# Kernel optimization log

Measured on AMD Instinct MI355X. Metric: run time of the kernel, lower is better.

Reference implementation:

```python
import jax, jax.numpy as jnp
import numpy as np

COMMITMENT = 0.25
EPS = 1e-12  # F.normalize default eps


def _l2norm(x, axis=-1):
    n = jnp.sqrt(jnp.sum(x * x, axis=axis, keepdims=True))
    return x / jnp.maximum(n, EPS)


def _wn(g, v):
    # torch weight_norm(Linear) with dim=0: per-output-row normalization
    return g[:, None] * v / jnp.maximum(jnp.sqrt(jnp.sum(v * v, axis=1, keepdims=True)), EPS)


def setup_inputs() -> dict:
    key = jax.random.key(0)
    ks = jax.random.split(key, 8)
    B, D, T = 16, 1024, 4096
    CS, CD = 1024, 8
    return {
        "z": jax.random.normal(ks[0], (B, D, T), dtype=jnp.float32),
        "codebook": jax.random.normal(ks[1], (CS, CD), dtype=jnp.float32),
        "g_in": jax.random.uniform(ks[2], (CD,), dtype=jnp.float32) + 0.5,
        "v_in": jax.random.normal(ks[3], (CD, D), dtype=jnp.float32) * 0.02,
        "b_in": jax.random.normal(ks[4], (CD,), dtype=jnp.float32) * 0.02,
        "g_out": jax.random.uniform(ks[5], (D,), dtype=jnp.float32) + 0.5,
        "v_out": jax.random.normal(ks[6], (D, CD), dtype=jnp.float32) * 0.02,
        "b_out": jax.random.normal(ks[7], (D,), dtype=jnp.float32) * 0.02,
    }


def reference(z, codebook, g_in, v_in, b_in, g_out, v_out, b_out):
    B, D, T = z.shape
    CS, CD = codebook.shape
    W_in = _wn(g_in, v_in)    # [CD, D]
    W_out = _wn(g_out, v_out)  # [D, CD]

    # in_proj: (b t d) @ W_in^T + b -> expressed directly on [B, D, T]
    z_e = jnp.einsum("bdt,cd->bct", z, W_in) + b_in[None, :, None]  # [B, CD, T]

    # decode_latents: cosine-distance nearest neighbor over codebook
    enc = z_e.transpose(0, 2, 1).reshape(B * T, CD)
    enc_n = _l2norm(enc)
    cb_n = _l2norm(codebook)
    dist = (
        jnp.sum(enc_n * enc_n, axis=1, keepdims=True)
        - 2.0 * enc_n @ cb_n.T
        + jnp.sum(cb_n * cb_n, axis=1)[None, :]
    )  # [B*T, CS]
    indices = jnp.argmax(-dist, axis=1).reshape(B, T)  # [B, T]

    # gather from the UN-normalized codebook (embed_code uses raw weights)
    z_q = codebook[indices].transpose(0, 2, 1)  # [B, CD, T]

    sg = jax.lax.stop_gradient
    commitment_loss = jnp.mean((z_e - sg(z_q)) ** 2, axis=(1, 2)) * COMMITMENT
    codebook_loss = jnp.mean((z_q - sg(z_e)) ** 2, axis=(1, 2))
    commit_loss = commitment_loss + codebook_loss  # [B]

    # straight-through estimator
    z_q_st = z_e + sg(z_q - z_e)  # [B, CD, T]

    out = jnp.einsum("bct,dc->bdt", z_q_st, W_out) + b_out[None, :, None]  # [B, D, T]
    return out, indices, commit_loss
```

## Files before the change

### kernel.cpp

```cpp
#include <hip/hip_runtime.h>
#include <math.h>
#include <stdint.h>

#define B_ 16
#define D_ 1024
#define T_ 4096
#define CS_ 1024
#define CD_ 8

__device__ __forceinline__ float f_tree8(const float r[8]) {
  return __fadd_rn(
      __fadd_rn(__fadd_rn(r[0], r[1]), __fadd_rn(r[2], r[3])),
      __fadd_rn(__fadd_rn(r[4], r[5]), __fadd_rn(r[6], r[7])));
}
__device__ __forceinline__ float f_sumsq8(const float x[8]) {
  float s[8];
#pragma unroll
  for (int k = 0; k < 8; ++k) s[k] = __fmul_rn(x[k], x[k]);
  return f_tree8(s);
}

__global__ __launch_bounds__(1024) void vq_setup(
    const float* __restrict__ cb, const float* __restrict__ g_in,
    const float* __restrict__ v_in, const float* __restrict__ g_out,
    const float* __restrict__ v_out, const float* __restrict__ b_out,
    double* __restrict__ WTd, float* __restrict__ cb16,
    float* __restrict__ wo16) {
  __shared__ float sv[8 * 1024];
  __shared__ float leafs[64];
  __shared__ float den[8];
  const int tid = threadIdx.x;

  for (int i = tid; i < 8 * 1024; i += 1024) sv[i] = v_in[i];
  __syncthreads();

  if (tid < 64) {
    const int c = tid >> 3, l = tid & 7;
    const float* a = sv + c * 1024 + l * 128;
    float r[8];
#pragma unroll
    for (int k = 0; k < 8; ++k) r[k] = __fmul_rn(a[k], a[k]);
    for (int i = 8; i < 128; i += 8) {
#pragma unroll
      for (int k = 0; k < 8; ++k)
        r[k] = __fadd_rn(r[k], __fmul_rn(a[i + k], a[i + k]));
    }
    leafs[c * 8 + l] = f_tree8(r);
  }
  __syncthreads();
  if (tid < 8) {
    const float* L = leafs + tid * 8;
    float lr[8];
#pragma unroll
    for (int k = 0; k < 8; ++k) lr[k] = L[k];
    const float s = f_tree8(lr);
    den[tid] = fmaxf(__fsqrt_rn(s), 1e-12f);
  }
  __syncthreads();

  if (tid < 1024) {
#pragma unroll
    for (int c = 0; c < 8; ++c) {
      const float w = __fdiv_rn(__fmul_rn(g_in[c], sv[c * 1024 + tid]), den[c]);
      WTd[tid * 8 + c] = (double)w;
    }
    {
      const float* cr = cb + tid * 8;
      float q[8];
#pragma unroll
      for (int c = 0; c < 8; ++c) q[c] = cr[c];
      const float nn = f_sumsq8(q);
      const float dd = fmaxf(__fsqrt_rn(nn), 1e-12f);
      float qn[8];
#pragma unroll
      for (int c = 0; c < 8; ++c) {
        qn[c] = __fdiv_rn(q[c], dd);
        cb16[tid * 16 + c] = qn[c];
      }
      cb16[tid * 16 + 8] = f_sumsq8(qn);
#pragma unroll
      for (int c = 9; c < 16; ++c) cb16[tid * 16 + c] = 0.f;
    }
    {
      const float* vr = v_out + tid * 8;
      float w[8];
#pragma unroll
      for (int c = 0; c < 8; ++c) w[c] = vr[c];
      const float n2 = f_sumsq8(w);
      const float d2 = fmaxf(__fsqrt_rn(n2), 1e-12f);
      const float go = g_out[tid];
#pragma unroll
      for (int c = 0; c < 8; ++c)
        wo16[tid * 16 + c] = __fdiv_rn(__fmul_rn(go, w[c]), d2);
      wo16[tid * 16 + 8] = b_out[tid];
#pragma unroll
      for (int c = 9; c < 16; ++c) wo16[tid * 16 + c] = 0.f;
    }
  }
}

__global__ __launch_bounds__(1024, 8) void vq_main(
    const float* __restrict__ z, const float* __restrict__ cbraw,
    const float* __restrict__ b_in, const double* __restrict__ WTd,
    const float* __restrict__ cb16, const float* __restrict__ wo16,
    float* __restrict__ out, float* __restrict__ oidx,
    float* __restrict__ lossp) {
  __shared__ double accb[8704];
  const int tid = threadIdx.x;
  const int q0 = __builtin_amdgcn_readfirstlane(tid >> 6);
  const int tl = tid & 63;
  const int blk = blockIdx.x;
  const int b = blk >> 5;
  const int tile = blk & 31;
  const int t0 = tile * 128 + tl * 2;

  const float2* zp2 =
      (const float2*)(z + ((size_t)b * D_ + (size_t)q0 * 64) * T_ + t0);
  const double* wd = WTd + (size_t)q0 * 512;

  double acc0[8], acc1[8];
#pragma unroll
  for (int c = 0; c < 8; ++c) { acc0[c] = 0.0; acc1[c] = 0.0; }

  float2 zA[4], zB[4];
#pragma unroll
  for (int u = 0; u < 4; ++u) zA[u] = zp2[(size_t)u * (T_ / 2)];

#pragma unroll
  for (int dc = 0; dc < 64; dc += 8) {
#pragma unroll
    for (int u = 0; u < 4; ++u)
      zB[u] = zp2[(size_t)(dc + 4 + u) * (T_ / 2)];
    __builtin_amdgcn_sched_barrier(0);
#pragma unroll
    for (int u = 0; u < 4; ++u) {
      const double* w = wd + (size_t)(dc + u) * 8;
      const double zx = (double)zA[u].x, zy = (double)zA[u].y;
#pragma unroll
      for (int c = 0; c < 8; ++c) {
        acc0[c] = fma(zx, w[c], acc0[c]);
        acc1[c] = fma(zy, w[c], acc1[c]);
      }
    }
    if (dc + 8 < 64) {
#pragma unroll
      for (int u = 0; u < 4; ++u)
        zA[u] = zp2[(size_t)(dc + 8 + u) * (T_ / 2)];
    }
    __builtin_amdgcn_sched_barrier(0);
#pragma unroll
    for (int u = 0; u < 4; ++u) {
      const double* w = wd + (size_t)(dc + 4 + u) * 8;
      const double zx = (double)zB[u].x, zy = (double)zB[u].y;
#pragma unroll
      for (int c = 0; c < 8; ++c) {
        acc0[c] = fma(zx, w[c], acc0[c]);
        acc1[c] = fma(zy, w[c], acc1[c]);
      }
    }
  }

  double2* accb2 = (double2*)accb;
  double2* totb = accb2 + 4096;
  double tot0[8], tot1[8];
#pragma unroll
  for (int half = 0; half < 2; ++half) {
    const int c0 = half * 4;
#pragma unroll
    for (int c = 0; c < 4; ++c) {
      double2 v; v.x = acc0[c0 + c]; v.y = acc1[c0 + c];
      accb2[c * 1024 + tid] = v;
    }
    __syncthreads();
    if (tid < 64) {
#pragma unroll
      for (int c = 0; c < 4; ++c) {
        const double2* row = accb2 + c * 1024 + tl;
        double2 s = row[0];
#pragma unroll
        for (int qq = 1; qq < 16; ++qq) {
          const double2 v = row[qq * 64];
          s.x = s.x + v.x;
          s.y = s.y + v.y;
        }
        totb[c * 64 + tl] = s;
      }
    }
    __syncthreads();
#pragma unroll
    for (int c = 0; c < 4; ++c) {
      const double2 s = totb[c * 64 + tl];
      tot0[c0 + c] = s.x; tot1[c0 + c] = s.y;
    }
  }

  float e0[8], e1[8], en0[8], en1[8];
#pragma unroll
  for (int c = 0; c < 8; ++c) {
    e0[c] = __fadd_rn((float)tot0[c], b_in[c]);
    e1[c] = __fadd_rn((float)tot1[c], b_in[c]);
  }
  const float n20 = f_sumsq8(e0), n21 = f_sumsq8(e1);
  const float dn0 = fmaxf(__fsqrt_rn(n20), 1e-12f);
  const float dn1 = fmaxf(__fsqrt_rn(n21), 1e-12f);
#pragma unroll
  for (int c = 0; c < 8; ++c) {
    en0[c] = __fdiv_rn(e0[c], dn0);
    en1[c] = __fdiv_rn(e1[c], dn1);
  }
  const float s_enc0 = f_sumsq8(en0), s_enc1 = f_sumsq8(en1);

  const int j0 = q0 * 64;
  float best0 = INFINITY, best1 = INFINITY;
  int bj0 = j0, bj1 = j0;
  {
    const float* cbq = cb16 + (size_t)j0 * 16;
#pragma unroll 4
    for (int jj = 0; jj < 64; ++jj) {
      const float* row = cbq + jj * 16;
      const float4 lo = *(const float4*)(row);
      const float4 hi = *(const float4*)(row + 4);
      const float sc = row[8];
      float d0 = 0.f, d1 = 0.f;
      d0 = fmaf(en0[0], lo.x, d0); d1 = fmaf(en1[0], lo.x, d1);
      d0 = fmaf(en0[1], lo.y, d0); d1 = fmaf(en1[1], lo.y, d1);
      d0 = fmaf(en0[2], lo.z, d0); d1 = fmaf(en1[2], lo.z, d1);
      d0 = fmaf(en0[3], lo.w, d0); d1 = fmaf(en1[3], lo.w, d1);
      d0 = fmaf(en0[4], hi.x, d0); d1 = fmaf(en1[4], hi.x, d1);
      d0 = fmaf(en0[5], hi.y, d0); d1 = fmaf(en1[5], hi.y, d1);
      d0 = fmaf(en0[6], hi.z, d0); d1 = fmaf(en1[6], hi.z, d1);
      d0 = fmaf(en0[7], hi.w, d0); d1 = fmaf(en1[7], hi.w, d1);
      const float dist0 =
          __fadd_rn(__fsub_rn(s_enc0, __fmul_rn(2.0f, d0)), sc);
      const float dist1 =
          __fadd_rn(__fsub_rn(s_enc1, __fmul_rn(2.0f, d1)), sc);
      if (dist0 < best0) { best0 = dist0; bj0 = j0 + jj; }
      if (dist1 < best1) { best1 = dist1; bj1 = j0 + jj; }
    }
  }

  float* distf0 = (float*)accb;
  int* candj0 = (int*)((char*)accb + 4096);
  float* distf1 = (float*)((char*)accb + 8192);
  int* candj1 = (int*)((char*)accb + 12288);
  int* ibuf = (int*)((char*)accb + 16384);
  distf0[tid] = best0; candj0[tid] = bj0;
  distf1[tid] = best1; candj1[tid] = bj1;
  __syncthreads();

  if (tid < 64) {
    float bd0 = distf0[tl], bd1 = distf1[tl];
    int ci0 = candj0[tl], ci1 = candj1[tl];
#pragma unroll
    for (int qq = 1; qq < 16; ++qq) {
      float dd = distf0[qq * 64 + tl];
      int jj = candj0[qq * 64 + tl];
      if (dd < bd0) { bd0 = dd; ci0 = jj; }
      dd = distf1[qq * 64 + tl];
      jj = candj1[qq * 64 + tl];
      if (dd < bd1) { bd1 = dd; ci1 = jj; }
    }
    ibuf[tl] = ci0; ibuf[64 + tl] = ci1;
    float2 iv; iv.x = (float)ci0; iv.y = (float)ci1;
    *(float2*)(oidx + (size_t)b * T_ + t0) = iv;
  }
  __syncthreads();
  const int bi0 = ibuf[tid & 63];
  const int bi1 = ibuf[64 + (tid & 63)];

  float cq0[8], cq1[8];
  {
    const float* cp0 = cbraw + (size_t)bi0 * 8;
    const float* cp1 = cbraw + (size_t)bi1 * 8;
#pragma unroll
    for (int c = 0; c < 8; ++c) { cq0[c] = cp0[c]; cq1[c] = cp1[c]; }
  }

  if (tid < 64) {
    float lsum = 0.f;
#pragma unroll
    for (int c = 0; c < 8; ++c) {
      const float df0 = __fsub_rn(e0[c], cq0[c]);
      lsum = fmaf(df0, df0, lsum);
    }
#pragma unroll
    for (int c = 0; c < 8; ++c) {
      const float df1 = __fsub_rn(e1[c], cq1[c]);
      lsum = fmaf(df1, df1, lsum);
    }
#pragma unroll
    for (int off = 32; off > 0; off >>= 1)
      lsum += __shfl_down(lsum, off, 64);
    if (tl == 0) lossp[blk] = lsum;
  }

  float2* op2 =
      (float2*)(out + ((size_t)b * D_ + (size_t)q0 * 64) * T_ + t0);
  const float* woq = wo16 + (size_t)q0 * 1024;
#pragma unroll 4
  for (int d = 0; d < 64; ++d) {
    const float* row = woq + d * 16;
    const float4 lo = *(const float4*)(row);
    const float4 hi = *(const float4*)(row + 4);
    const float bo = row[8];
    float d0 = 0.f, d1 = 0.f;
    d0 = fmaf(cq0[0], lo.x, d0); d1 = fmaf(cq1[0], lo.x, d1);
    d0 = fmaf(cq0[1], lo.y, d0); d1 = fmaf(cq1[1], lo.y, d1);
    d0 = fmaf(cq0[2], lo.z, d0); d1 = fmaf(cq1[2], lo.z, d1);
    d0 = fmaf(cq0[3], lo.w, d0); d1 = fmaf(cq1[3], lo.w, d1);
    d0 = fmaf(cq0[4], hi.x, d0); d1 = fmaf(cq1[4], hi.x, d1);
    d0 = fmaf(cq0[5], hi.y, d0); d1 = fmaf(cq1[5], hi.y, d1);
    d0 = fmaf(cq0[6], hi.z, d0); d1 = fmaf(cq1[6], hi.z, d1);
    d0 = fmaf(cq0[7], hi.w, d0); d1 = fmaf(cq1[7], hi.w, d1);
    float2 ov; ov.x = __fadd_rn(d0, bo); ov.y = __fadd_rn(d1, bo);
    op2[(size_t)d * (T_ / 2)] = ov;
  }
}

__global__ __launch_bounds__(64) void vq_fin(const float* __restrict__ lossp,
                                             float* __restrict__ oloss) {
  const int tid = threadIdx.x;
  if (tid < B_) {
    float s = 0.f;
    for (int i = 0; i < 32; ++i) s += lossp[tid * 32 + i];
    oloss[tid] = s * (1.25f / 32768.0f);
  }
}

extern "C" void kernel_launch(void* const* d_in, const int* in_sizes, int n_in,
                              void* d_out, int out_size, void* d_ws,
                              size_t ws_size, hipStream_t stream) {
  (void)in_sizes; (void)n_in; (void)out_size; (void)ws_size;
  const float* z = (const float*)d_in[0];
  const float* cb = (const float*)d_in[1];
  const float* g_in = (const float*)d_in[2];
  const float* v_in = (const float*)d_in[3];
  const float* b_in = (const float*)d_in[4];
  const float* g_out = (const float*)d_in[5];
  const float* v_out = (const float*)d_in[6];
  const float* b_out = (const float*)d_in[7];
  float* out = (float*)d_out;

  char* ws = (char*)d_ws;
  double* WTd = (double*)ws;
  float* cb16 = (float*)(ws + 65536);
  float* wo16 = (float*)(ws + 131072);
  float* lossp = (float*)(ws + 196608);

  float* oidx = out + (size_t)B_ * D_ * T_;
  float* oloss = oidx + (size_t)B_ * T_;

  vq_setup<<<1, 1024, 0, stream>>>(cb, g_in, v_in, g_out, v_out, b_out, WTd,
                                   cb16, wo16);
  vq_main<<<512, 1024, 0, stream>>>(z, cb, b_in, WTd, cb16, wo16, out, oidx,
                                    lossp);
  vq_fin<<<1, 64, 0, stream>>>(lossp, oloss);
}
```

Baseline: 158.8 us.

## Process four timesteps per thread with float4 loads and halve the grid

```diff
diff --git a/kernel.cpp b/kernel.cpp
--- a/kernel.cpp
+++ b/kernel.cpp
@@ -99,7 +99,7 @@
   }
 }
 
-__global__ __launch_bounds__(1024, 8) void vq_main(
+__global__ __launch_bounds__(1024, 4) void vq_main(
     const float* __restrict__ z, const float* __restrict__ cbraw,
     const float* __restrict__ b_in, const double* __restrict__ WTd,
     const float* __restrict__ cb16, const float* __restrict__ wo16,
@@ -110,72 +110,81 @@
   const int q0 = __builtin_amdgcn_readfirstlane(tid >> 6);
   const int tl = tid & 63;
   const int blk = blockIdx.x;
-  const int b = blk >> 5;
-  const int tile = blk & 31;
-  const int t0 = tile * 128 + tl * 2;
-
-  const float2* zp2 =
-      (const float2*)(z + ((size_t)b * D_ + (size_t)q0 * 64) * T_ + t0);
+  const int b = blk >> 4;
+  const int tile = blk & 15;
+  const int t0 = tile * 256 + tl * 4;
+
+  const float4* zp4 =
+      (const float4*)(z + ((size_t)b * D_ + (size_t)q0 * 64) * T_ + t0);
   const double* wd = WTd + (size_t)q0 * 512;
 
-  double acc0[8], acc1[8];
-#pragma unroll
-  for (int c = 0; c < 8; ++c) { acc0[c] = 0.0; acc1[c] = 0.0; }
-
-  float2 zA[4], zB[4];
-#pragma unroll
-  for (int u = 0; u < 4; ++u) zA[u] = zp2[(size_t)u * (T_ / 2)];
+  double a0[8], a1[8], a2[8], a3[8];
+#pragma unroll
+  for (int c = 0; c < 8; ++c) { a0[c] = 0.0; a1[c] = 0.0; a2[c] = 0.0; a3[c] = 0.0; }
+
+  float4 zA[4], zB[4];
+#pragma unroll
+  for (int u = 0; u < 4; ++u) zA[u] = zp4[(size_t)u * (T_ / 4)];
 
 #pragma unroll
   for (int dc = 0; dc < 64; dc += 8) {
 #pragma unroll
     for (int u = 0; u < 4; ++u)
-      zB[u] = zp2[(size_t)(dc + 4 + u) * (T_ / 2)];
-    __builtin_amdgcn_sched_barrier(0);
+      zB[u] = zp4[(size_t)(dc + 4 + u) * (T_ / 4)];
 #pragma unroll
     for (int u = 0; u < 4; ++u) {
       const double* w = wd + (size_t)(dc + u) * 8;
       const double zx = (double)zA[u].x, zy = (double)zA[u].y;
+      const double zz = (double)zA[u].z, zw = (double)zA[u].w;
 #pragma unroll
       for (int c = 0; c < 8; ++c) {
-        acc0[c] = fma(zx, w[c], acc0[c]);
-        acc1[c] = fma(zy, w[c], acc1[c]);
+        a0[c] = fma(zx, w[c], a0[c]);
+        a1[c] = fma(zy, w[c], a1[c]);
+        a2[c] = fma(zz, w[c], a2[c]);
+        a3[c] = fma(zw, w[c], a3[c]);
       }
     }
     if (dc + 8 < 64) {
 #pragma unroll
       for (int u = 0; u < 4; ++u)
-        zA[u] = zp2[(size_t)(dc + 8 + u) * (T_ / 2)];
-    }
-    __builtin_amdgcn_sched_barrier(0);
+        zA[u] = zp4[(size_t)(dc + 8 + u) * (T_ / 4)];
+    }
 #pragma unroll
     for (int u = 0; u < 4; ++u) {
       const double* w = wd + (size_t)(dc + 4 + u) * 8;
       const double zx = (double)zB[u].x, zy = (double)zB[u].y;
+      const double zz = (double)zB[u].z, zw = (double)zB[u].w;
 #pragma unroll
       for (int c = 0; c < 8; ++c) {
-        acc0[c] = fma(zx, w[c], acc0[c]);
-        acc1[c] = fma(zy, w[c], acc1[c]);
+        a0[c] = fma(zx, w[c], a0[c]);
+        a1[c] = fma(zy, w[c], a1[c]);
+        a2[c] = fma(zz, w[c], a2[c]);
+        a3[c] = fma(zw, w[c], a3[c]);
       }
     }
   }
 
   double2* accb2 = (double2*)accb;
   double2* totb = accb2 + 4096;
-  double tot0[8], tot1[8];
-#pragma unroll
-  for (int half = 0; half < 2; ++half) {
-    const int c0 = half * 4;
-#pragma unroll
-    for (int c = 0; c < 4; ++c) {
-      double2 v; v.x = acc0[c0 + c]; v.y = acc1[c0 + c];
-      accb2[c * 1024 + tid] = v;
+  double t_0[8], t_1[8], t_2[8], t_3[8];
+#pragma unroll
+  for (int pass = 0; pass < 4; ++pass) {
+    const int c0 = pass * 2;
+#pragma unroll
+    for (int cc = 0; cc < 2; ++cc) {
+      double2 p01, p23;
+      p01.x = (cc ? a0[c0 + 1] : a0[c0]);
+      p01.y = (cc ? a1[c0 + 1] : a1[c0]);
+      p23.x = (cc ? a2[c0 + 1] : a2[c0]);
+      p23.y = (cc ? a3[c0 + 1] : a3[c0]);
+      accb2[(cc * 2 + 0) * 1024 + tid] = p01;
+      accb2[(cc * 2 + 1) * 1024 + tid] = p23;
     }
     __syncthreads();
     if (tid < 64) {
 #pragma unroll
-      for (int c = 0; c < 4; ++c) {
-        const double2* row = accb2 + c * 1024 + tl;
+      for (int r = 0; r < 4; ++r) {
+        const double2* row = accb2 + r * 1024 + tl;
         double2 s = row[0];
 #pragma unroll
         for (int qq = 1; qq < 16; ++qq) {
@@ -183,36 +192,45 @@
           s.x = s.x + v.x;
           s.y = s.y + v.y;
         }
-        totb[c * 64 + tl] = s;
+        totb[r * 64 + tl] = s;
       }
     }
     __syncthreads();
 #pragma unroll
-    for (int c = 0; c < 4; ++c) {
-      const double2 s = totb[c * 64 + tl];
-      tot0[c0 + c] = s.x; tot1[c0 + c] = s.y;
-    }
-  }
-
-  float e0[8], e1[8], en0[8], en1[8];
+    for (int cc = 0; cc < 2; ++cc) {
+      const double2 s01 = totb[(cc * 2 + 0) * 64 + tl];
+      const double2 s23 = totb[(cc * 2 + 1) * 64 + tl];
+      t_0[c0 + cc] = s01.x; t_1[c0 + cc] = s01.y;
+      t_2[c0 + cc] = s23.x; t_3[c0 + cc] = s23.y;
+    }
+    __syncthreads();
+  }
+
+  float e0[8], e1[8], e2[8], e3[8], en0[8], en1[8], en2[8], en3[8];
 #pragma unroll
   for (int c = 0; c < 8; ++c) {
-    e0[c] = __fadd_rn((float)tot0[c], b_in[c]);
-    e1[c] = __fadd_rn((float)tot1[c], b_in[c]);
-  }
-  const float n20 = f_sumsq8(e0), n21 = f_sumsq8(e1);
-  const float dn0 = fmaxf(__fsqrt_rn(n20), 1e-12f);
-  const float dn1 = fmaxf(__fsqrt_rn(n21), 1e-12f);
+    e0[c] = __fadd_rn((float)t_0[c], b_in[c]);
+    e1[c] = __fadd_rn((float)t_1[c], b_in[c]);
+    e2[c] = __fadd_rn((float)t_2[c], b_in[c]);
+    e3[c] = __fadd_rn((float)t_3[c], b_in[c]);
+  }
+  const float dn0 = fmaxf(__fsqrt_rn(f_sumsq8(e0)), 1e-12f);
+  const float dn1 = fmaxf(__fsqrt_rn(f_sumsq8(e1)), 1e-12f);
+  const float dn2 = fmaxf(__fsqrt_rn(f_sumsq8(e2)), 1e-12f);
+  const float dn3 = fmaxf(__fsqrt_rn(f_sumsq8(e3)), 1e-12f);
 #pragma unroll
   for (int c = 0; c < 8; ++c) {
     en0[c] = __fdiv_rn(e0[c], dn0);
     en1[c] = __fdiv_rn(e1[c], dn1);
-  }
-  const float s_enc0 = f_sumsq8(en0), s_enc1 = f_sumsq8(en1);
+    en2[c] = __fdiv_rn(e2[c], dn2);
+    en3[c] = __fdiv_rn(e3[c], dn3);
+  }
+  const float se0 = f_sumsq8(en0), se1 = f_sumsq8(en1);
+  const float se2 = f_sumsq8(en2), se3 = f_sumsq8(en3);
 
   const int j0 = q0 * 64;
-  float best0 = INFINITY, best1 = INFINITY;
-  int bj0 = j0, bj1 = j0;
+  float b0 = INFINITY, b1 = INFINITY, b2 = INFINITY, b3 = INFINITY;
+  int j_0 = j0, j_1 = j0, j_2 = j0, j_3 = j0;
   {
     const float* cbq = cb16 + (size_t)j0 * 16;
 #pragma unroll 4
@@ -221,72 +239,96 @@
       const float4 lo = *(const float4*)(row);
       const float4 hi = *(const float4*)(row + 4);
       const float sc = row[8];
-      float d0 = 0.f, d1 = 0.f;
+      float d0 = 0.f, d1 = 0.f, d2 = 0.f, d3 = 0.f;
       d0 = fmaf(en0[0], lo.x, d0); d1 = fmaf(en1[0], lo.x, d1);
+      d2 = fmaf(en2[0], lo.x, d2); d3 = fmaf(en3[0], lo.x, d3);
       d0 = fmaf(en0[1], lo.y, d0); d1 = fmaf(en1[1], lo.y, d1);
+      d2 = fmaf(en2[1], lo.y, d2); d3 = fmaf(en3[1], lo.y, d3);
       d0 = fmaf(en0[2], lo.z, d0); d1 = fmaf(en1[2], lo.z, d1);
+      d2 = fmaf(en2[2], lo.z, d2); d3 = fmaf(en3[2], lo.z, d3);
       d0 = fmaf(en0[3], lo.w, d0); d1 = fmaf(en1[3], lo.w, d1);
+      d2 = fmaf(en2[3], lo.w, d2); d3 = fmaf(en3[3], lo.w, d3);
       d0 = fmaf(en0[4], hi.x, d0); d1 = fmaf(en1[4], hi.x, d1);
+      d2 = fmaf(en2[4], hi.x, d2); d3 = fmaf(en3[4], hi.x, d3);
       d0 = fmaf(en0[5], hi.y, d0); d1 = fmaf(en1[5], hi.y, d1);
+      d2 = fmaf(en2[5], hi.y, d2); d3 = fmaf(en3[5], hi.y, d3);
       d0 = fmaf(en0[6], hi.z, d0); d1 = fmaf(en1[6], hi.z, d1);
+      d2 = fmaf(en2[6], hi.z, d2); d3 = fmaf(en3[6], hi.z, d3);
       d0 = fmaf(en0[7], hi.w, d0); d1 = fmaf(en1[7], hi.w, d1);
-      const float dist0 =
-          __fadd_rn(__fsub_rn(s_enc0, __fmul_rn(2.0f, d0)), sc);
-      const float dist1 =
-          __fadd_rn(__fsub_rn(s_enc1, __fmul_rn(2.0f, d1)), sc);
-      if (dist0 < best0) { best0 = dist0; bj0 = j0 + jj; }
-      if (dist1 < best1) { best1 = dist1; bj1 = j0 + jj; }
-    }
-  }
-
-  float* distf0 = (float*)accb;
-  int* candj0 = (int*)((char*)accb + 4096);
-  float* distf1 = (float*)((char*)accb + 8192);
-  int* candj1 = (int*)((char*)accb + 12288);
-  int* ibuf = (int*)((char*)accb + 16384);
-  distf0[tid] = best0; candj0[tid] = bj0;
-  distf1[tid] = best1; candj1[tid] = bj1;
+      d2 = fmaf(en2[7], hi.w, d2); d3 = fmaf(en3[7], hi.w, d3);
+      const float x0 = __fadd_rn(__fsub_rn(se0, __fmul_rn(2.0f, d0)), sc);
+      const float x1 = __fadd_rn(__fsub_rn(se1, __fmul_rn(2.0f, d1)), sc);
+      const float x2 = __fadd_rn(__fsub_rn(se2, __fmul_rn(2.0f, d2)), sc);
+      const float x3 = __fadd_rn(__fsub_rn(se3, __fmul_rn(2.0f, d3)), sc);
+      if (x0 < b0) { b0 = x0; j_0 = j0 + jj; }
+      if (x1 < b1) { b1 = x1; j_1 = j0 + jj; }
+      if (x2 < b2) { b2 = x2; j_2 = j0 + jj; }
+      if (x3 < b3) { b3 = x3; j_3 = j0 + jj; }
+    }
+  }
+
+  float* df = (float*)accb;
+  int* cj = (int*)((char*)accb + 16384);
+  int* ibuf = (int*)((char*)accb + 32768);
+  df[tid] = b0; df[1024 + tid] = b1; df[2048 + tid] = b2; df[3072 + tid] = b3;
+  cj[tid] = j_0; cj[1024 + tid] = j_1; cj[2048 + tid] = j_2; cj[3072 + tid] = j_3;
   __syncthreads();
 
   if (tid < 64) {
-    float bd0 = distf0[tl], bd1 = distf1[tl];
-    int ci0 = candj0[tl], ci1 = candj1[tl];
-#pragma unroll
-    for (int qq = 1; qq < 16; ++qq) {
-      float dd = distf0[qq * 64 + tl];
-      int jj = candj0[qq * 64 + tl];
-      if (dd < bd0) { bd0 = dd; ci0 = jj; }
-      dd = distf1[qq * 64 + tl];
-      jj = candj1[qq * 64 + tl];
-      if (dd < bd1) { bd1 = dd; ci1 = jj; }
-    }
-    ibuf[tl] = ci0; ibuf[64 + tl] = ci1;
-    float2 iv; iv.x = (float)ci0; iv.y = (float)ci1;
-    *(float2*)(oidx + (size_t)b * T_ + t0) = iv;
+    int win[4];
+#pragma unroll
+    for (int k = 0; k < 4; ++k) {
+      const float* dk = df + k * 1024;
+      const int* jk = cj + k * 1024;
+      float bd = dk[tl];
+      int bi = jk[tl];
+#pragma unroll
+      for (int qq = 1; qq < 16; ++qq) {
+        const float dd = dk[qq * 64 + tl];
+        const int jv = jk[qq * 64 + tl];
+        if (dd < bd) { bd = dd; bi = jv; }
+      }
+      win[k] = bi;
+      ibuf[k * 64 + tl] = bi;
+    }
+    float4 iv;
+    iv.x = (float)win[0]; iv.y = (float)win[1];
+    iv.z = (float)win[2]; iv.w = (float)win[3];
+    *(float4*)(oidx + (size_t)b * T_ + t0) = iv;
   }
   __syncthreads();
-  const int bi0 = ibuf[tid & 63];
-  const int bi1 = ibuf[64 + (tid & 63)];
-
-  float cq0[8], cq1[8];
+  const int bi0 = ibuf[tl], bi1 = ibuf[64 + tl];
+  const int bi2 = ibuf[128 + tl], bi3 = ibuf[192 + tl];
+
+  float cq0[8], cq1[8], cq2[8], cq3[8];
   {
-    const float* cp0 = cbraw + (size_t)bi0 * 8;
-    const float* cp1 = cbraw + (size_t)bi1 * 8;
-#pragma unroll
-    for (int c = 0; c < 8; ++c) { cq0[c] = cp0[c]; cq1[c] = cp1[c]; }
+    const float* p0 = cbraw + (size_t)bi0 * 8;
+    const float* p1 = cbraw + (size_t)bi1 * 8;
+    const float* p2 = cbraw + (size_t)bi2 * 8;
+    const float* p3 = cbraw + (size_t)bi3 * 8;
+#pragma unroll
+    for (int c = 0; c < 8; ++c) {
+      cq0[c] = p0[c]; cq1[c] = p1[c]; cq2[c] = p2[c]; cq3[c] = p3[c];
+    }
   }
 
   if (tid < 64) {
     float lsum = 0.f;
 #pragma unroll
     for (int c = 0; c < 8; ++c) {
-      const float df0 = __fsub_rn(e0[c], cq0[c]);
-      lsum = fmaf(df0, df0, lsum);
-    }
-#pragma unroll
-    for (int c = 0; c < 8; ++c) {
-      const float df1 = __fsub_rn(e1[c], cq1[c]);
-      lsum = fmaf(df1, df1, lsum);
+      const float f0 = __fsub_rn(e0[c], cq0[c]); lsum = fmaf(f0, f0, lsum);
+    }
+#pragma unroll
+    for (int c = 0; c < 8; ++c) {
+      const float f1 = __fsub_rn(e1[c], cq1[c]); lsum = fmaf(f1, f1, lsum);
+    }
+#pragma unroll
+    for (int c = 0; c < 8; ++c) {
+      const float f2 = __fsub_rn(e2[c], cq2[c]); lsum = fmaf(f2, f2, lsum);
+    }
+#pragma unroll
+    for (int c = 0; c < 8; ++c) {
+      const float f3 = __fsub_rn(e3[c], cq3[c]); lsum = fmaf(f3, f3, lsum);
     }
 #pragma unroll
     for (int off = 32; off > 0; off >>= 1)
@@ -294,8 +336,8 @@
     if (tl == 0) lossp[blk] = lsum;
   }
 
-  float2* op2 =
-      (float2*)(out + ((size_t)b * D_ + (size_t)q0 * 64) * T_ + t0);
+  float4* op4 =
+      (float4*)(out + ((size_t)b * D_ + (size_t)q0 * 64) * T_ + t0);
   const float* woq = wo16 + (size_t)q0 * 1024;
 #pragma unroll 4
   for (int d = 0; d < 64; ++d) {
@@ -303,17 +345,27 @@
     const float4 lo = *(const float4*)(row);
     const float4 hi = *(const float4*)(row + 4);
     const float bo = row[8];
-    float d0 = 0.f, d1 = 0.f;
+    float d0 = 0.f, d1 = 0.f, d2 = 0.f, d3 = 0.f;
     d0 = fmaf(cq0[0], lo.x, d0); d1 = fmaf(cq1[0], lo.x, d1);
+    d2 = fmaf(cq2[0], lo.x, d2); d3 = fmaf(cq3[0], lo.x, d3);
     d0 = fmaf(cq0[1], lo.y, d0); d1 = fmaf(cq1[1], lo.y, d1);
+    d2 = fmaf(cq2[1], lo.y, d2); d3 = fmaf(cq3[1], lo.y, d3);
     d0 = fmaf(cq0[2], lo.z, d0); d1 = fmaf(cq1[2], lo.z, d1);
+    d2 = fmaf(cq2[2], lo.z, d2); d3 = fmaf(cq3[2], lo.z, d3);
     d0 = fmaf(cq0[3], lo.w, d0); d1 = fmaf(cq1[3], lo.w, d1);
+    d2 = fmaf(cq2[3], lo.w, d2); d3 = fmaf(cq3[3], lo.w, d3);
     d0 = fmaf(cq0[4], hi.x, d0); d1 = fmaf(cq1[4], hi.x, d1);
+    d2 = fmaf(cq2[4], hi.x, d2); d3 = fmaf(cq3[4], hi.x, d3);
     d0 = fmaf(cq0[5], hi.y, d0); d1 = fmaf(cq1[5], hi.y, d1);
+    d2 = fmaf(cq2[5], hi.y, d2); d3 = fmaf(cq3[5], hi.y, d3);
     d0 = fmaf(cq0[6], hi.z, d0); d1 = fmaf(cq1[6], hi.z, d1);
+    d2 = fmaf(cq2[6], hi.z, d2); d3 = fmaf(cq3[6], hi.z, d3);
     d0 = fmaf(cq0[7], hi.w, d0); d1 = fmaf(cq1[7], hi.w, d1);
-    float2 ov; ov.x = __fadd_rn(d0, bo); ov.y = __fadd_rn(d1, bo);
-    op2[(size_t)d * (T_ / 2)] = ov;
+    d2 = fmaf(cq2[7], hi.w, d2); d3 = fmaf(cq3[7], hi.w, d3);
+    float4 ov;
+    ov.x = __fadd_rn(d0, bo); ov.y = __fadd_rn(d1, bo);
+    ov.z = __fadd_rn(d2, bo); ov.w = __fadd_rn(d3, bo);
+    op4[(size_t)d * (T_ / 4)] = ov;
   }
 }
 
@@ -322,7 +374,7 @@
   const int tid = threadIdx.x;
   if (tid < B_) {
     float s = 0.f;
-    for (int i = 0; i < 32; ++i) s += lossp[tid * 32 + i];
+    for (int i = 0; i < 16; ++i) s += lossp[tid * 16 + i];
     oloss[tid] = s * (1.25f / 32768.0f);
   }
 }
@@ -352,7 +404,7 @@
 
   vq_setup<<<1, 1024, 0, stream>>>(cb, g_in, v_in, g_out, v_out, b_out, WTd,
                                    cb16, wo16);
-  vq_main<<<512, 1024, 0, stream>>>(z, cb, b_in, WTd, cb16, wo16, out, oidx,
+  vq_main<<<256, 1024, 0, stream>>>(z, cb, b_in, WTd, cb16, wo16, out, oidx,
                                     lossp);
   vq_fin<<<1, 64, 0, stream>>>(lossp, oloss);
 }
```

Result: slower. 167.9 us (+5.7%).
